# Performance work log

Measured on AMD Instinct MI355X. Metric: run time of the kernel, lower is better.

## Reference

```python
import jax, jax.numpy as jnp
import numpy as np

LN_EPS = 1e-5


def layer_norm(x, g, b):
    m = jnp.mean(x, axis=-1, keepdims=True)
    v = jnp.mean(jnp.square(x - m), axis=-1, keepdims=True)
    return (x - m) * jax.lax.rsqrt(v + LN_EPS) * g + b


def sym_norm(A):
    # D^{-1/2} (A + I) D^{-1/2}
    N = A.shape[0]
    Ah = A + jnp.eye(N, dtype=A.dtype)
    d = jnp.sum(Ah, axis=-1)
    dinv = jax.lax.rsqrt(jnp.maximum(d, 1e-12))
    return Ah * dinv[:, None] * dinv[None, :]


def gru_layer(xs, Wih, Whh, bih, bhh):
    # xs: (BN, T, Din) -> ys: (BN, T, H). PyTorch GRU cell math.
    BN, T, _ = xs.shape
    H = Whh.shape[1]
    x_proj = xs @ Wih.T + bih  # (BN, T, 3H), precompute input projections

    def step(h, xp):
        hp = h @ Whh.T + bhh
        xr, xz, xn = jnp.split(xp, 3, axis=-1)
        hr, hz, hn = jnp.split(hp, 3, axis=-1)
        r = jax.nn.sigmoid(xr + hr)
        z = jax.nn.sigmoid(xz + hz)
        n = jnp.tanh(xn + r * hn)
        h_new = (1.0 - z) * n + z * h
        return h_new, h_new

    h0 = jnp.zeros((BN, H), xs.dtype)
    _, ys = jax.lax.scan(step, h0, jnp.swapaxes(x_proj, 0, 1))
    return jnp.swapaxes(ys, 0, 1)


def amscf_forward(x, A, FSP, DSP,
                  E1, E2, fus_W, fus_b, fus_v, beta1, beta2,
                  gcn_W1, gcn_b1, ln1_g, ln1_b, gcn_W2, gcn_b2, ln2_g, ln2_b,
                  gru_Wih0, gru_Whh0, gru_bih0, gru_bhh0,
                  gru_Wih1, gru_Whh1, gru_bih1, gru_bhh1,
                  att_w, fc1_W, fc1_b, fc2_W, fc2_b):
    B, T, N, _ = x.shape
    Hor = fc2_W.shape[0]

    # ImprovedAdjacency: blend A with adaptive node-embedding adjacency
    Aadp = jax.nn.softmax(jax.nn.relu(E1 @ E2.T), axis=-1)
    IA = 0.5 * A + 0.5 * Aadp

    # fuse_with_A with learned gates
    w1 = jax.nn.sigmoid(beta1)
    w2 = jax.nn.sigmoid(beta2)
    C1 = w1 * A + (1.0 - w1) * FSP
    C2 = w2 * A + (1.0 - w2) * DSP

    # TransposeAttentionFusion: graph-level attention over the 3 candidate graphs
    Gs = jnp.stack([IA, C1, C2], axis=0)  # (3, N, N)
    sc = jnp.mean(jnp.tanh(Gs @ fus_W.T + fus_b) @ fus_v, axis=-1)  # (3,)
    alpha = jax.nn.softmax(sc)
    MG = jnp.einsum('k,knm->nm', alpha, Gs)

    S_hat = sym_norm(MG)  # (N, N)

    # TwoLayerGCN over all (B, T) at once: act(LN(S X W1)) -> LN(S h W2)
    xf = x.reshape(B * T, N, 1)
    h = jnp.einsum('mn,bnc->bmc', S_hat, xf) @ gcn_W1 + gcn_b1
    h = jax.nn.relu(layer_norm(h, ln1_g, ln1_b))
    g = jnp.einsum('mn,bnc->bmc', S_hat, h) @ gcn_W2 + gcn_b2
    g = layer_norm(g, ln2_g, ln2_b)  # (B*T, N, C)

    C = g.shape[-1]
    # Faithful to original: raw view of (B, T, N, C) into (B*N, T, C)
    H_seq = g.reshape(B, T, N, C).reshape(B * N, T, C)

    out = gru_layer(H_seq, gru_Wih0, gru_Whh0, gru_bih0, gru_bhh0)
    out = gru_layer(out, gru_Wih1, gru_Whh1, gru_bih1, gru_bhh1)  # (BN, T, Hg)

    # SoftAttentionPooling over time
    score = out @ att_w  # (BN, T)
    att = jax.nn.softmax(score, axis=1)
    ctx = jnp.einsum('bt,bth->bh', att, out)

    hfc = jax.nn.gelu(ctx @ fc1_W.T + fc1_b)
    dlt = hfc @ fc2_W.T + fc2_b  # (BN, Hor); dropout is identity at eval
    return jnp.transpose(dlt.reshape(B, N, Hor), (0, 2, 1))  # (B, Hor, N)


def setup_inputs() -> dict:
    B, T, N, Hor = 32, 12, 1000, 12
    Cin, Ch, Cout, Hg, Da, De = 1, 96, 96, 192, 32, 10
    key = jax.random.key(0)
    ks = jax.random.split(key, 32)
    f32 = jnp.float32

    def nrm(k, shape, scale):
        return jax.random.normal(k, shape, dtype=f32) * scale

    inp = {
        'x': jax.random.normal(ks[0], (B, T, N, Cin), dtype=f32),
        'A': jax.random.uniform(ks[1], (N, N), dtype=f32),
        'FSP': jax.random.uniform(ks[2], (N, N), dtype=f32),
        'DSP': jax.random.uniform(ks[3], (N, N), dtype=f32),
        'E1': nrm(ks[4], (N, De), 0.1),
        'E2': nrm(ks[5], (N, De), 0.1),
        'fus_W': nrm(ks[6], (Da, N), 1.0 / np.sqrt(N)),
        'fus_b': jnp.zeros((Da,), f32),
        'fus_v': nrm(ks[7], (Da,), 1.0 / np.sqrt(Da)),
        'beta1': jnp.float32(0.5),
        'beta2': jnp.float32(0.5),
        'gcn_W1': nrm(ks[8], (Cin, Ch), 1.0 / np.sqrt(Cin)),
        'gcn_b1': jnp.zeros((Ch,), f32),
        'ln1_g': jnp.ones((Ch,), f32),
        'ln1_b': jnp.zeros((Ch,), f32),
        'gcn_W2': nrm(ks[9], (Ch, Cout), 1.0 / np.sqrt(Ch)),
        'gcn_b2': jnp.zeros((Cout,), f32),
        'ln2_g': jnp.ones((Cout,), f32),
        'ln2_b': jnp.zeros((Cout,), f32),
        'gru_Wih0': nrm(ks[10], (3 * Hg, Cout), 1.0 / np.sqrt(Hg)),
        'gru_Whh0': nrm(ks[11], (3 * Hg, Hg), 1.0 / np.sqrt(Hg)),
        'gru_bih0': jnp.zeros((3 * Hg,), f32),
        'gru_bhh0': jnp.zeros((3 * Hg,), f32),
        'gru_Wih1': nrm(ks[12], (3 * Hg, Hg), 1.0 / np.sqrt(Hg)),
        'gru_Whh1': nrm(ks[13], (3 * Hg, Hg), 1.0 / np.sqrt(Hg)),
        'gru_bih1': jnp.zeros((3 * Hg,), f32),
        'gru_bhh1': jnp.zeros((3 * Hg,), f32),
        'att_w': nrm(ks[14], (Hg,), 1.0 / np.sqrt(Hg)),
        'fc1_W': nrm(ks[15], (Hg, Hg), 1.0 / np.sqrt(Hg)),
        'fc1_b': jnp.zeros((Hg,), f32),
        'fc2_W': nrm(ks[16], (Hor, Hg), 1.0 / np.sqrt(Hg)),
        'fc2_b': jnp.zeros((Hor,), f32),
    }
    return inp


def reference(x, A, FSP, DSP, E1, E2, fus_W, fus_b, fus_v, beta1, beta2,
              gcn_W1, gcn_b1, ln1_g, ln1_b, gcn_W2, gcn_b2, ln2_g, ln2_b,
              gru_Wih0, gru_Whh0, gru_bih0, gru_bhh0,
              gru_Wih1, gru_Whh1, gru_bih1, gru_bhh1,
              att_w, fc1_W, fc1_b, fc2_W, fc2_b):
    return amscf_forward(x, A, FSP, DSP, E1, E2, fus_W, fus_b, fus_v, beta1, beta2,
                         gcn_W1, gcn_b1, ln1_g, ln1_b, gcn_W2, gcn_b2, ln2_g, ln2_b,
                         gru_Wih0, gru_Whh0, gru_bih0, gru_bhh0,
                         gru_Wih1, gru_Whh1, gru_bih1, gru_bhh1,
                         att_w, fc1_W, fc1_b, fc2_W, fc2_b)
```

## Files before the change

### kernel.cpp

```cpp
#include <hip/hip_runtime.h>

typedef unsigned short u16;
typedef unsigned int u32;
typedef __attribute__((ext_vector_type(8))) short short8;
typedef __attribute__((ext_vector_type(4))) float float4v;

#define DEV static __device__ __forceinline__

DEV float bf2f(u16 u) { u32 x = ((u32)u) << 16; float f; __builtin_memcpy(&f, &x, 4); return f; }
DEV u16 f2bf(float f) {
  u32 u; __builtin_memcpy(&u, &f, 4);
  u = (u + 0x7fffu + ((u >> 16) & 1u)) >> 16;
  return (u16)u;
}
DEV float sigm(float x) { return 1.f / (1.f + __expf(-x)); }

DEV void gl16(const u16* g, u16* l) {
  __builtin_amdgcn_global_load_lds(
      (const __attribute__((address_space(1))) void*)g,
      (__attribute__((address_space(3))) void*)l, 16, 0, 0);
}

template <int OMODE>
__launch_bounds__(256)
__global__ void gemm_nt(const u16* __restrict__ A, int lda,
                        const u16* __restrict__ B, int ldb,
                        void* __restrict__ Cp, int ldc,
                        int M, int N, int K,
                        const float* __restrict__ bias)
{
  constexpr int PK = 40;
  __shared__ u16 As[128 * PK];
  __shared__ u16 Bs[64 * PK];

  const int tid  = threadIdx.x;
  const int m0   = blockIdx.y * 128;
  const int n0   = blockIdx.x * 64;
  const int wid  = tid >> 6;
  const int lane = tid & 63;
  const int l15  = lane & 15;
  const int quad = lane >> 4;
  const int wm   = (wid >> 1) * 64;
  const int wn   = (wid & 1) * 32;

  float4v acc[4][2];
  const float4v fz = {0.f, 0.f, 0.f, 0.f};
#pragma unroll
  for (int i = 0; i < 4; i++)
#pragma unroll
    for (int j = 0; j < 2; j++) acc[i][j] = fz;

  const int arow = tid >> 2;
  const int akc  = tid & 3;

  const int kt_count = (K + 31) / 32;
  for (int kt = 0; kt < kt_count; ++kt) {
    const int k0 = kt * 32 + akc * 8;
    const bool kok = (k0 < K);
    uint4 av0 = make_uint4(0, 0, 0, 0), av1 = av0, bv = av0;
    int ra = m0 + arow;
    if (kok && ra < M)        av0 = *(const uint4*)(A + (size_t)ra * lda + k0);
    if (kok && ra + 64 < M)   av1 = *(const uint4*)(A + (size_t)(ra + 64) * lda + k0);
    int rb = n0 + arow;
    if (kok && rb < N)        bv  = *(const uint4*)(B + (size_t)rb * ldb + k0);

    __syncthreads();
    *(uint4*)&As[arow * PK + akc * 8]        = av0;
    *(uint4*)&As[(arow + 64) * PK + akc * 8] = av1;
    *(uint4*)&Bs[arow * PK + akc * 8]        = bv;
    __syncthreads();

    short8 af[4], bfr[2];
#pragma unroll
    for (int i = 0; i < 4; i++)
      af[i] = *(const short8*)&As[(wm + i * 16 + l15) * PK + quad * 8];
#pragma unroll
    for (int j = 0; j < 2; j++)
      bfr[j] = *(const short8*)&Bs[(wn + j * 16 + l15) * PK + quad * 8];
#pragma unroll
    for (int i = 0; i < 4; i++)
#pragma unroll
      for (int j = 0; j < 2; j++)
        acc[i][j] = __builtin_amdgcn_mfma_f32_16x16x32_bf16(af[i], bfr[j], acc[i][j], 0, 0, 0);
  }

#pragma unroll
  for (int i = 0; i < 4; i++)
#pragma unroll
    for (int j = 0; j < 2; j++)
#pragma unroll
      for (int e = 0; e < 4; e++) {
        int r = m0 + wm + i * 16 + quad * 4 + e;
        int c = n0 + wn + j * 16 + l15;
        if (r < M && c < N) {
          float v = acc[i][j][e];
          if (OMODE == 0) ((float*)Cp)[(size_t)r * ldc + c] = v;
          else {
            float a = v + bias[c];
            float t = tanhf(0.7978845608028654f * (a + 0.044715f * a * a * a));
            ((float*)Cp)[(size_t)r * ldc + c] = 0.5f * a * (1.f + t);
          }
        }
      }
}

__launch_bounds__(256)
__global__ void k_bigemm(const u16* __restrict__ A,
                         const u16* __restrict__ B,
                         u16* __restrict__ Gg)
{
  __shared__ u16 As[128 * 32];
  __shared__ u16 Bs[128 * 32];
  const int tid  = threadIdx.x;
  const int bid  = blockIdx.x;
  const int xcd  = bid & 7;
  const int jj   = bid >> 3;
  const int m0   = (jj & 7) * 128;
  const int n0   = (xcd + 8 * (jj >> 3)) * 128;

  const int wid  = tid >> 6;
  const int lane = tid & 63;
  const int l15  = lane & 15;
  const int quad = lane >> 4;
  const int wm   = (wid >> 1) * 64;
  const int wn   = (wid & 1) * 64;

  const int srow = wid * 16 + (lane >> 2);
  const int skc  = (((lane & 3) ^ ((lane >> 2) & 3))) * 8;

  const u16* agp0 = A + (size_t)(m0 + srow) * 1024 + skc;
  const u16* agp1 = agp0 + (size_t)64 * 1024;
  const u16* bgp0 = B + (size_t)(n0 + srow) * 1024 + skc;
  const u16* bgp1 = bgp0 + (size_t)64 * 1024;
  u16* asl0 = &As[(wid * 16) * 32];
  u16* asl1 = &As[(64 + wid * 16) * 32];
  u16* bsl0 = &Bs[(wid * 16) * 32];
  u16* bsl1 = &Bs[(64 + wid * 16) * 32];

  float4v acc[4][4];
  const float4v fz = {0.f, 0.f, 0.f, 0.f};
#pragma unroll
  for (int i = 0; i < 4; i++)
#pragma unroll
    for (int j = 0; j < 4; j++) acc[i][j] = fz;

  const int swa = (quad ^ (l15 & 3)) * 8;

  for (int kt = 0; kt < 32; ++kt) {
    const int ko = kt * 32;
    gl16(agp0 + ko, asl0);
    gl16(agp1 + ko, asl1);
    gl16(bgp0 + ko, bsl0);
    gl16(bgp1 + ko, bsl1);
    __syncthreads();
    short8 af[4], bf[4];
#pragma unroll
    for (int i = 0; i < 4; i++)
      af[i] = *(const short8*)&As[(wm + i * 16 + l15) * 32 + swa];
#pragma unroll
    for (int j = 0; j < 4; j++)
      bf[j] = *(const short8*)&Bs[(wn + j * 16 + l15) * 32 + swa];
#pragma unroll
    for (int i = 0; i < 4; i++)
#pragma unroll
      for (int j = 0; j < 4; j++)
        acc[i][j] = __builtin_amdgcn_mfma_f32_16x16x32_bf16(af[i], bf[j], acc[i][j], 0, 0, 0);
    __syncthreads();
  }

#pragma unroll
  for (int i = 0; i < 4; i++)
#pragma unroll
    for (int j = 0; j < 4; j++)
#pragma unroll
      for (int e = 0; e < 4; e++) {
        int r = m0 + wm + i * 16 + quad * 4 + e;
        if (r < 1000) {
          int c = n0 + wn + j * 16 + l15;
          int rs = c / 96, cc = c - rs * 96;
          Gg[(size_t)rs * 96000 + (size_t)r * 96 + cc] = f2bf(acc[i][j][e]);
        }
      }
}

template <int KX, bool POOL>
__launch_bounds__(256)
__global__ void k_gru(const u16* __restrict__ Xin, int ldx,
                      const u16* __restrict__ Win,
                      const u16* __restrict__ Hin,
                      const u16* __restrict__ Whh,
                      const float* __restrict__ bih, const float* __restrict__ bhh,
                      u16* __restrict__ Hout,
                      const float* __restrict__ att_w, float* __restrict__ score,
                      int t0)
{
  __shared__ u16 As[128 * 64];
  __shared__ u16 Bs[96 * 64];
  const int tid  = threadIdx.x;
  const int m0   = blockIdx.y * 128;
  const int c0   = blockIdx.x * 32;
  const int wid  = tid >> 6;
  const int lane = tid & 63;
  const int l15  = lane & 15;
  const int quad = lane >> 4;
  const int wm   = wid * 32;

  const int srow8 = lane >> 3;
  const int sw8   = ((lane & 7) ^ srow8) * 8;
  const int srow4 = lane >> 2;
  const int sw4   = (((lane & 3) ^ (srow4 & 3))) * 8;

  float4v aR[2][2], aZ[2][2], aXN[2][2], aHN[2][2];
  const float4v fz = {0.f, 0.f, 0.f, 0.f};
#pragma unroll
  for (int i = 0; i < 2; i++)
#pragma unroll
    for (int j = 0; j < 2; j++) { aR[i][j] = fz; aZ[i][j] = fz; aXN[i][j] = fz; aHN[i][j] = fz; }

  if (KX == 96) {
    const u16* ax0 = Xin + (size_t)(m0 + wid * 16 + srow4) * ldx + sw4;
    const u16* ax1 = Xin + (size_t)(m0 + 64 + wid * 16 + srow4) * ldx + sw4;
    const int b0 = wid * 16 + srow4;
    const u16* bx0 = Win + (size_t)((b0 >> 5) * 192 + c0 + (b0 & 31)) * 96 + sw4;
    const int b1 = 64 + wid * 16 + srow4;
    const u16* bx1 = Win + (size_t)(384 + c0 + (b1 & 31)) * 96 + sw4;
    u16* asl0 = &As[(wid * 16) * 32];
    u16* asl1 = &As[(64 + wid * 16) * 32];
    u16* bsl0 = &Bs[(wid * 16) * 32];
    u16* bsl1 = &Bs[(64 + wid * 16) * 32];
    const int swa = (quad ^ (l15 & 3)) * 8;
#pragma unroll
    for (int kt = 0; kt < 3; ++kt) {
      const int ko = kt * 32;
      gl16(ax0 + ko, asl0); gl16(ax1 + ko, asl1);
      gl16(bx0 + ko, bsl0);
      if (wid < 2) gl16(bx1 + ko, bsl1);
      __syncthreads();
      short8 af[2], bR[2], bZ[2], bN[2];
#pragma unroll
      for (int i = 0; i < 2; i++)
        af[i] = *(const short8*)&As[(wm + i * 16 + l15) * 32 + swa];
#pragma unroll
      for (int j = 0; j < 2; j++) {
        bR[j] = *(const short8*)&Bs[(j * 16 + l15) * 32 + swa];
        bZ[j] = *(const short8*)&Bs[(32 + j * 16 + l15) * 32 + swa];
        bN[j] = *(const short8*)&Bs[(64 + j * 16 + l15) * 32 + swa];
      }
#pragma unroll
      for (int i = 0; i < 2; i++)
#pragma unroll
        for (int j = 0; j < 2; j++) {
          aR[i][j]  = __builtin_amdgcn_mfma_f32_16x16x32_bf16(af[i], bR[j], aR[i][j], 0, 0, 0);
          aZ[i][j]  = __builtin_amdgcn_mfma_f32_16x16x32_bf16(af[i], bZ[j], aZ[i][j], 0, 0, 0);
          aXN[i][j] = __builtin_amdgcn_mfma_f32_16x16x32_bf16(af[i], bN[j], aXN[i][j], 0, 0, 0);
        }
      __syncthreads();
    }
  } else {
    const u16* abase = Xin + (size_t)(m0 + wid * 8 + srow8) * 192 + sw8;
    const u16* bbase = Win + (size_t)(c0 + wid * 8 + srow8) * 192 + sw8;
#pragma unroll
    for (int kt = 0; kt < 3; ++kt) {
      const int ko = kt * 64;
#pragma unroll
      for (int c = 0; c < 4; c++)
        gl16(abase + (size_t)c * 32 * 192 + ko, &As[(c * 32 + wid * 8) * 64]);
#pragma unroll
      for (int c = 0; c < 3; c++)
        gl16(bbase + (size_t)c * 192 * 192 + ko, &Bs[(c * 32 + wid * 8) * 64]);
      __syncthreads();
#pragma unroll
      for (int k32 = 0; k32 < 2; k32++) {
        const int swr = ((quad + 4 * k32) ^ (l15 & 7)) * 8;
        short8 af[2], bR[2], bZ[2], bN[2];
#pragma unroll
        for (int i = 0; i < 2; i++)
          af[i] = *(const short8*)&As[(wm + i * 16 + l15) * 64 + swr];
#pragma unroll
        for (int j = 0; j < 2; j++) {
          bR[j] = *(const short8*)&Bs[(j * 16 + l15) * 64 + swr];
          bZ[j] = *(const short8*)&Bs[(32 + j * 16 + l15) * 64 + swr];
          bN[j] = *(const short8*)&Bs[(64 + j * 16 + l15) * 64 + swr];
        }
#pragma unroll
        for (int i = 0; i < 2; i++)
#pragma unroll
          for (int j = 0; j < 2; j++) {
            aR[i][j]  = __builtin_amdgcn_mfma_f32_16x16x32_bf16(af[i], bR[j], aR[i][j], 0, 0, 0);
            aZ[i][j]  = __builtin_amdgcn_mfma_f32_16x16x32_bf16(af[i], bZ[j], aZ[i][j], 0, 0, 0);
            aXN[i][j] = __builtin_amdgcn_mfma_f32_16x16x32_bf16(af[i], bN[j], aXN[i][j], 0, 0, 0);
          }
      }
      __syncthreads();
    }
  }
  if (!t0) {
    const u16* abase = Hin + (size_t)(m0 + wid * 8 + srow8) * 192 + sw8;
    const u16* bbase = Whh + (size_t)(c0 + wid * 8 + srow8) * 192 + sw8;
#pragma unroll
    for (int kt = 0; kt < 3; ++kt) {
      const int ko = kt * 64;
#pragma unroll
      for (int c = 0; c < 4; c++)
        gl16(abase + (size_t)c * 32 * 192 + ko, &As[(c * 32 + wid * 8) * 64]);
#pragma unroll
      for (int c = 0; c < 3; c++)
        gl16(bbase + (size_t)c * 192 * 192 + ko, &Bs[(c * 32 + wid * 8) * 64]);
      __syncthreads();
#pragma unroll
      for (int k32 = 0; k32 < 2; k32++) {
        const int swr = ((quad + 4 * k32) ^ (l15 & 7)) * 8;
        short8 af[2], bR[2], bZ[2], bN[2];
#pragma unroll
        for (int i = 0; i < 2; i++)
          af[i] = *(const short8*)&As[(wm + i * 16 + l15) * 64 + swr];
#pragma unroll
        for (int j = 0; j < 2; j++) {
          bR[j] = *(const short8*)&Bs[(j * 16 + l15) * 64 + swr];
          bZ[j] = *(const short8*)&Bs[(32 + j * 16 + l15) * 64 + swr];
          bN[j] = *(const short8*)&Bs[(64 + j * 16 + l15) * 64 + swr];
        }
#pragma unroll
        for (int i = 0; i < 2; i++)
#pragma unroll
          for (int j = 0; j < 2; j++) {
            aR[i][j]  = __builtin_amdgcn_mfma_f32_16x16x32_bf16(af[i], bR[j], aR[i][j], 0, 0, 0);
            aZ[i][j]  = __builtin_amdgcn_mfma_f32_16x16x32_bf16(af[i], bZ[j], aZ[i][j], 0, 0, 0);
            aHN[i][j] = __builtin_amdgcn_mfma_f32_16x16x32_bf16(af[i], bN[j], aHN[i][j], 0, 0, 0);
          }
      }
      __syncthreads();
    }
  }

  float ps[2][4];
  if (POOL) {
#pragma unroll
    for (int i = 0; i < 2; i++)
#pragma unroll
      for (int e = 0; e < 4; e++) ps[i][e] = 0.f;
  }
#pragma unroll
  for (int j = 0; j < 2; ++j) {
    const int c = c0 + j * 16 + l15;
    const float brz = bih[c] + bhh[c];
    const float bzz = bih[192 + c] + bhh[192 + c];
    const float bxn = bih[384 + c];
    const float bhn = bhh[384 + c];
    const float aw  = POOL ? att_w[c] : 0.f;
#pragma unroll
    for (int i = 0; i < 2; ++i)
#pragma unroll
      for (int e = 0; e < 4; ++e) {
        const int row = m0 + wm + i * 16 + quad * 4 + e;
        float rg  = sigm(aR[i][j][e] + brz);
        float zg  = sigm(aZ[i][j][e] + bzz);
        float hnv = bhn + (t0 ? 0.f : aHN[i][j][e]);
        float ng  = tanhf(aXN[i][j][e] + bxn + rg * hnv);
        float hold = t0 ? 0.f : bf2f(Hin[(size_t)row * 192 + c]);
        float hnew = (1.f - zg) * ng + zg * hold;
        Hout[(size_t)row * 192 + c] = f2bf(hnew);
        if (POOL) ps[i][e] += hnew * aw;
      }
  }
  if (POOL) {
#pragma unroll
    for (int i = 0; i < 2; ++i)
#pragma unroll
      for (int e = 0; e < 4; ++e) {
        float v = ps[i][e];
        v += __shfl_xor(v, 1); v += __shfl_xor(v, 2);
        v += __shfl_xor(v, 4); v += __shfl_xor(v, 8);
        if (l15 == 0) atomicAdd(&score[m0 + wm + i * 16 + quad * 4 + e], v);
      }
  }
}

__launch_bounds__(256)
__global__ void k_pool(const u16* __restrict__ H, float* __restrict__ score,
                       float* __restrict__ Mbuf, float* __restrict__ Lbuf,
                       float* __restrict__ Nv, int t0)
{
  const int base = blockIdx.x * 1536;
  const int tid  = threadIdx.x;

  float prev[6], hnew[6], so[6], wn[6];
#pragma unroll
  for (int k = 0; k < 6; k++) {
    const int idx = base + tid + k * 256;
    const int q = idx / 192;
    const float s = score[q];
    hnew[k] = bf2f(H[idx]);
    if (t0) {
      so[k] = 0.f; wn[k] = 1.f; prev[k] = 0.f;
    } else {
      const float Mo = Mbuf[q];
      const float Mn = fmaxf(Mo, s);
      so[k] = __expf(Mo - Mn);
      wn[k] = __expf(s - Mn);
      prev[k] = Nv[idx];
    }
  }
  float Mw = 0.f, Lw = 0.f;
  int qw = -1;
  if (tid < 8) {
    qw = blockIdx.x * 8 + tid;
    const float s = score[qw];
    if (t0) { Mw = s; Lw = 1.f; }
    else {
      const float Mo = Mbuf[qw];
      const float Mn = fmaxf(Mo, s);
      Mw = Mn;
      Lw = Lbuf[qw] * __expf(Mo - Mn) + __expf(s - Mn);
    }
  }
  __syncthreads();
  if (tid < 8) { Mbuf[qw] = Mw; Lbuf[qw] = Lw; score[qw] = 0.f; }
#pragma unroll
  for (int k = 0; k < 6; k++) {
    const int idx = base + tid + k * 256;
    Nv[idx] = prev[k] * so[k] + wn[k] * hnew[k];
  }
}

__launch_bounds__(256)
__global__ void k_h2gemm(const float* __restrict__ yt, const float4* __restrict__ cwpk,
                         const u16* __restrict__ W2s, const float* __restrict__ consts,
                         u16* __restrict__ h2t)
{
  constexpr int PK = 40;
  __shared__ u16 As[128 * PK];
  __shared__ u16 Bs[96 * PK];
  __shared__ u16 Ts[96 * 136];

  const int tid  = threadIdx.x;
  const int m0   = blockIdx.x * 128;
  const int wid  = tid >> 6;
  const int lane = tid & 63;
  const int l15  = lane & 15;
  const int quad = lane >> 4;
  const int wm   = (wid >> 1) * 64;
  const int wn   = (wid & 1) * 48;

  const float P = consts[0], Q = consts[1], VW = consts[2], CWB = consts[3], VB = consts[4];

  const int arow = tid >> 2;
  const int akc  = tid & 3;

  float yv[2], mu[2], iv[2];
#pragma unroll
  for (int rr = 0; rr < 2; rr++) {
    int i = m0 + arow + rr * 64;
    int r = i / 1000, n = i - r * 1000;
    float y = yt[n * 384 + r];
    yv[rr] = y;
    mu[rr] = y * P + Q;
    iv[rr] = rsqrtf(y * y * VW + 2.f * y * CWB + VB + 1e-5f);
  }

  float4v acc[4][3];
  const float4v fz = {0.f, 0.f, 0.f, 0.f};
#pragma unroll
  for (int i = 0; i < 4; i++)
#pragma unroll
    for (int j = 0; j < 3; j++) acc[i][j] = fz;

  uint4 asave[2][3];
  const bool has2 = (arow < 32);

  for (int kt = 0; kt < 6; ++kt) {
    const int k0 = kt * 32 + akc * 8;
    uint4 av[2];
    if (kt < 3) {
#pragma unroll
      for (int rr = 0; rr < 2; rr++) {
        u16 hb[8];
#pragma unroll
        for (int e = 0; e < 8; e++) {
          float4 cw = cwpk[k0 + e];
          float t = yv[rr] * cw.x + cw.y - mu[rr];
          float h = fmaxf(t * iv[rr] * cw.z + cw.w, 0.f);
          hb[e] = f2bf(h);
        }
        __builtin_memcpy(&av[rr], hb, 16);
        asave[rr][kt] = av[rr];
      }
    } else {
      av[0] = asave[0][kt - 3];
      av[1] = asave[1][kt - 3];
    }
    uint4 bv0 = *(const uint4*)(W2s + (size_t)arow * 192 + k0);
    uint4 bv1 = make_uint4(0, 0, 0, 0);
    if (has2) bv1 = *(const uint4*)(W2s + (size_t)(arow + 64) * 192 + k0);

    __syncthreads();
    *(uint4*)&As[arow * PK + akc * 8]        = av[0];
    *(uint4*)&As[(arow + 64) * PK + akc * 8] = av[1];
    *(uint4*)&Bs[arow * PK + akc * 8]        = bv0;
    if (has2) *(uint4*)&Bs[(arow + 64) * PK + akc * 8] = bv1;
    __syncthreads();

    short8 af[4], bfr[3];
#pragma unroll
    for (int i = 0; i < 4; i++)
      af[i] = *(const short8*)&As[(wm + i * 16 + l15) * PK + quad * 8];
#pragma unroll
    for (int j = 0; j < 3; j++)
      bfr[j] = *(const short8*)&Bs[(wn + j * 16 + l15) * PK + quad * 8];
#pragma unroll
    for (int i = 0; i < 4; i++)
#pragma unroll
      for (int j = 0; j < 3; j++)
        acc[i][j] = __builtin_amdgcn_mfma_f32_16x16x32_bf16(af[i], bfr[j], acc[i][j], 0, 0, 0);
  }

#pragma unroll
  for (int i = 0; i < 4; i++)
#pragma unroll
    for (int j = 0; j < 3; j++)
#pragma unroll
      for (int e = 0; e < 4; e++) {
        int rowl = wm + i * 16 + quad * 4 + e;
        int c2   = wn + j * 16 + l15;
        Ts[c2 * 136 + rowl] = f2bf(acc[i][j][e]);
      }
  __syncthreads();
#pragma unroll
  for (int u = tid; u < 1536; u += 256) {
    int c2 = u >> 4, ch = u & 15;
    int iidx0 = m0 + ch * 8;
    int r = iidx0 / 1000, n0 = iidx0 - r * 1000;
    *(uint4*)(h2t + (size_t)(r * 96 + c2) * 1024 + n0) = *(const uint4*)&Ts[c2 * 136 + ch * 8];
  }
}

__launch_bounds__(256)
__global__ void k_prep(const float* x, const float* fus_W,
                       const float* Wih0, const float* Whh0,
                       const float* Wih1, const float* Whh1,
                       const float* gcn_W1, const float* gcn_b1,
                       const float* gcn_W2, const float* ln1g, const float* ln1b,
                       u16* xbf, u16* fusWbf, u16* Wih0b, u16* Whh0b, u16* Wih1b, u16* Whh1b,
                       u16* W2s, float4* cwpk, float* consts)
{
  long o = (long)blockIdx.x * 256 + threadIdx.x;
  if (o < 384000) xbf[o] = f2bf(x[o]);
  else if ((o -= 384000) < 32000) fusWbf[o] = f2bf(fus_W[o]);
  else if ((o -= 32000) < 55296)  Wih0b[o] = f2bf(Wih0[o]);
  else if ((o -= 55296) < 110592) Whh0b[o] = f2bf(Whh0[o]);
  else if ((o -= 110592) < 110592) Wih1b[o] = f2bf(Wih1[o]);
  else if ((o -= 110592) < 110592) Whh1b[o] = f2bf(Whh1[o]);
  else if ((o -= 110592) < 9216) {
    int c2 = (int)o / 96, c = (int)o - c2 * 96;
    float wv = gcn_W2[c * 96 + c2];
    u16 hi = f2bf(wv);
    u16 lo = f2bf(wv - bf2f(hi));
    W2s[c2 * 192 + c] = hi;
    W2s[c2 * 192 + 96 + c] = lo;
  }
  else if ((o -= 9216) < 96) {
    int c = (int)o;
    float4 cw;
    cw.x = gcn_W1[c]; cw.y = gcn_b1[c]; cw.z = ln1g[c]; cw.w = ln1b[c];
    cwpk[c] = cw;
  }
  if (blockIdx.x == 0 && threadIdx.x == 0) {
    float sw = 0, sb = 0, sww = 0, swb = 0, sbb = 0;
    for (int c = 0; c < 96; c++) {
      float wv = gcn_W1[c], b = gcn_b1[c];
      sw += wv; sb += b; sww += wv * wv; swb += wv * b; sbb += b * b;
    }
    float P = sw / 96.f, Q = sb / 96.f;
    consts[0] = P; consts[1] = Q;
    consts[2] = sww / 96.f - P * P;
    consts[3] = swb / 96.f - P * Q;
    consts[4] = sbb / 96.f - Q * Q;
  }
}

__launch_bounds__(256)
__global__ void k_zero(u16* __restrict__ h2t, float* __restrict__ score)
{
  int idx = blockIdx.x * 256 + threadIdx.x;
  if (idx < 110592) {
    int row = idx / 3, p = idx - row * 3;
    *(uint4*)(h2t + (size_t)row * 1024 + 1000 + p * 8) = make_uint4(0, 0, 0, 0);
  } else if ((idx -= 110592) < 32000) {
    score[idx] = 0.f;
  }
}

__launch_bounds__(256)
__global__ void k_w1split(const float* __restrict__ fc1W, u16* __restrict__ w1s)
{
  int idx = blockIdx.x * 256 + threadIdx.x;
  if (idx >= 192 * 192) return;
  int n = idx / 192, k = idx - n * 192;
  float w = fc1W[idx];
  u16 hi = f2bf(w);
  u16 lo = f2bf(w - bf2f(hi));
  w1s[(size_t)n * 576 + k]       = hi;
  w1s[(size_t)n * 576 + 192 + k] = lo;
  w1s[(size_t)n * 576 + 384 + k] = hi;
}

__launch_bounds__(256)
__global__ void k_adjrow(const float* __restrict__ A, const float* __restrict__ FSP,
                         const float* __restrict__ DSP, const float* __restrict__ E1,
                         const float* __restrict__ E2,
                         const float* beta1, const float* beta2,
                         u16* __restrict__ G, float* __restrict__ rowsums)
{
  __shared__ float z[1000];
  __shared__ float red[256];
  const int n = blockIdx.x, tid = threadIdx.x;

  float e1r[10];
#pragma unroll
  for (int d = 0; d < 10; d++) e1r[d] = E1[n * 10 + d];

  float lmax = -1e30f;
  for (int m = tid; m < 1000; m += 256) {
    float s = 0;
#pragma unroll
    for (int d = 0; d < 10; d++) s += e1r[d] * E2[m * 10 + d];
    s = fmaxf(s, 0.f);
    z[m] = s;
    lmax = fmaxf(lmax, s);
  }
  red[tid] = lmax; __syncthreads();
  for (int st = 128; st > 0; st >>= 1) { if (tid < st) red[tid] = fmaxf(red[tid], red[tid + st]); __syncthreads(); }
  const float mx = red[0]; __syncthreads();

  float lsum = 0;
  for (int m = tid; m < 1000; m += 256) { float e = __expf(z[m] - mx); z[m] = e; lsum += e; }
  red[tid] = lsum; __syncthreads();
  for (int st = 128; st > 0; st >>= 1) { if (tid < st) red[tid] += red[tid + st]; __syncthreads(); }
  const float inv = 1.f / red[0]; __syncthreads();

  const float w1 = sigm(beta1[0]);
  const float w2 = sigm(beta2[0]);
  float s0 = 0, s1 = 0, s2 = 0;
  for (int m = tid; m < 1000; m += 256) {
    float aadp = z[m] * inv;
    float a = A[n * 1000 + m], f = FSP[n * 1000 + m], dd = DSP[n * 1000 + m];
    float g0 = 0.5f * a + 0.5f * aadp;
    float g1 = w1 * a + (1.f - w1) * f;
    float g2 = w2 * a + (1.f - w2) * dd;
    G[0 * 1000000 + n * 1000 + m] = f2bf(g0);
    G[1 * 1000000 + n * 1000 + m] = f2bf(g1);
    G[2 * 1000000 + n * 1000 + m] = f2bf(g2);
    s0 += g0; s1 += g1; s2 += g2;
  }
  red[tid] = s0; __syncthreads();
  for (int st = 128; st > 0; st >>= 1) { if (tid < st) red[tid] += red[tid + st]; __syncthreads(); }
  if (tid == 0) rowsums[n] = red[0];
  __syncthreads();
  red[tid] = s1; __syncthreads();
  for (int st = 128; st > 0; st >>= 1) { if (tid < st) red[tid] += red[tid + st]; __syncthreads(); }
  if (tid == 0) rowsums[1000 + n] = red[0];
  __syncthreads();
  red[tid] = s2; __syncthreads();
  for (int st = 128; st > 0; st >>= 1) { if (tid < st) red[tid] += red[tid + st]; __syncthreads(); }
  if (tid == 0) rowsums[2000 + n] = red[0];
}

__launch_bounds__(256)
__global__ void k_sc(const float* __restrict__ P, const float* fus_b, const float* fus_v, float* sc)
{
  __shared__ float red[256];
  const int k = blockIdx.x, tid = threadIdx.x;
  float local = 0;
  for (int n = tid; n < 1000; n += 256) {
    const float* p = P + (size_t)(k * 1000 + n) * 32;
    float s = 0;
#pragma unroll
    for (int a = 0; a < 32; a++) s += tanhf(p[a] + fus_b[a]) * fus_v[a];
    local += s;
  }
  red[tid] = local; __syncthreads();
  for (int st = 128; st > 0; st >>= 1) { if (tid < st) red[tid] += red[tid + st]; __syncthreads(); }
  if (tid == 0) sc[k] = red[0] * (1.f / 1000.f);
}

__launch_bounds__(256)
__global__ void k_alpha(const float* sc, const float* rowsums, float* alpha_out, float* dinv)
{
  __shared__ float al[3];
  const int tid = threadIdx.x;
  if (tid == 0) {
    float m = fmaxf(sc[0], fmaxf(sc[1], sc[2]));
    float e0 = __expf(sc[0] - m), e1 = __expf(sc[1] - m), e2 = __expf(sc[2] - m);
    float inv = 1.f / (e0 + e1 + e2);
    al[0] = e0 * inv; al[1] = e1 * inv; al[2] = e2 * inv;
    alpha_out[0] = al[0]; alpha_out[1] = al[1]; alpha_out[2] = al[2];
  }
  __syncthreads();
  const float a0 = al[0], a1 = al[1], a2 = al[2];
  for (int n = tid; n < 1000; n += 256) {
    float d = a0 * rowsums[n] + a1 * rowsums[1000 + n] + a2 * rowsums[2000 + n] + 1.0f;
    dinv[n] = rsqrtf(fmaxf(d, 1e-12f));
  }
}

__launch_bounds__(256)
__global__ void k_shat(const u16* __restrict__ G, const float* alpha, const float* dinv,
                       u16* __restrict__ S)
{
  int idx = blockIdx.x * 256 + threadIdx.x;
  if (idx >= 1024000) return;
  int i = idx >> 10, j = idx & 1023;
  u16 val = 0;
  if (j < 1000) {
    const float a0 = alpha[0], a1 = alpha[1], a2 = alpha[2];
    int g = i * 1000 + j;
    float mg = a0 * bf2f(G[g]) + a1 * bf2f(G[1000000 + g]) + a2 * bf2f(G[2000000 + g]);
    if (i == j) mg += 1.0f;
    val = f2bf(mg * dinv[i] * dinv[j]);
  }
  S[(size_t)i * 1024 + j] = val;
}

__launch_bounds__(256)
__global__ void k_ln2g(u16* __restrict__ g, const float* __restrict__ b2,
                       const float* __restrict__ g2, const float* __restrict__ be2)
{
  const int i = blockIdx.x * 256 + threadIdx.x;
  if (i >= 384000) return;
  u16* row = g + (size_t)i * 96;

  uint4 raw[12];
#pragma unroll
  for (int t = 0; t < 12; t++) raw[t] = *(const uint4*)((const u16*)row + t * 8);

  float s = 0, ss = 0;
#pragma unroll
  for (int t = 0; t < 12; t++) {
    const u16* ch = (const u16*)&raw[t];
#pragma unroll
    for (int e = 0; e < 8; e++) {
      float v = bf2f(ch[e]) + b2[t * 8 + e];
      s += v; ss += v * v;
    }
  }
  const float mean = s * (1.f / 96.f);
  const float var  = ss * (1.f / 96.f) - mean * mean;
  const float isd  = rsqrtf(var + 1e-5f);

#pragma unroll
  for (int t = 0; t < 12; t++) {
    const u16* ch = (const u16*)&raw[t];
#pragma unroll
    for (int p = 0; p < 2; p++) {
      int c0 = t * 8 + p * 4;
      u32 w0 = f2bf((bf2f(ch[p * 4 + 0]) + b2[c0 + 0] - mean) * isd * g2[c0 + 0] + be2[c0 + 0]);
      u32 w1 = f2bf((bf2f(ch[p * 4 + 1]) + b2[c0 + 1] - mean) * isd * g2[c0 + 1] + be2[c0 + 1]);
      u32 w2 = f2bf((bf2f(ch[p * 4 + 2]) + b2[c0 + 2] - mean) * isd * g2[c0 + 2] + be2[c0 + 2]);
      u32 w3 = f2bf((bf2f(ch[p * 4 + 3]) + b2[c0 + 3] - mean) * isd * g2[c0 + 3] + be2[c0 + 3]);
      ((u32*)row)[t * 4 + p * 2 + 0] = (w0 | (w1 << 16));
      ((u32*)row)[t * 4 + p * 2 + 1] = (w2 | (w3 << 16));
    }
  }
}

__launch_bounds__(256)
__global__ void k_ctxsplit(const float* __restrict__ Nv, const float* __restrict__ Lbuf,
                           u16* __restrict__ ctxs)
{
  const int i = blockIdx.x * 256 + threadIdx.x;
  if (i >= 32000 * 192) return;
  const int q = i / 192, c = i - q * 192;
  float v = Nv[i] / Lbuf[q];
  u16 hi = f2bf(v);
  u16 lo = f2bf(v - bf2f(hi));
  u16* row = ctxs + (size_t)q * 576;
  row[c] = hi; row[192 + c] = hi; row[384 + c] = lo;
}

__launch_bounds__(192)
__global__ void k_fc2(const float* __restrict__ hfc, const float* __restrict__ fc2W,
                      const float* __restrict__ fc2b, float* __restrict__ out)
{
  __shared__ float w2S[12][193];
  __shared__ float hS[16][193];
  const int tid = threadIdx.x;
  const int q0 = blockIdx.x * 16;
  for (int idx = tid; idx < 12 * 192; idx += 192) {
    int o = idx / 192, k = idx - o * 192;
    w2S[o][k] = fc2W[idx];
  }
  for (int idx = tid; idx < 16 * 192; idx += 192) {
    int qq = idx / 192, k = idx - qq * 192;
    hS[qq][k] = hfc[(size_t)(q0 + qq) * 192 + k];
  }
  __syncthreads();
  const int qq = tid / 12, o = tid - qq * 12;
  float acc = fc2b[o];
#pragma unroll 8
  for (int k = 0; k < 192; k++) acc += hS[qq][k] * w2S[o][k];
  const int q = q0 + qq;
  const int b = q / 1000, node = q - b * 1000;
  out[(size_t)b * 12000 + o * 1000 + node] = acc;
}

extern "C" void kernel_launch(void* const* d_in, const int* in_sizes, int n_in,
                              void* d_out, int out_size, void* d_ws, size_t ws_size,
                              hipStream_t stream)
{
  const float* x     = (const float*)d_in[0];
  const float* A     = (const float*)d_in[1];
  const float* FSP   = (const float*)d_in[2];
  const float* DSP   = (const float*)d_in[3];
  const float* E1    = (const float*)d_in[4];
  const float* E2    = (const float*)d_in[5];
  const float* fus_W = (const float*)d_in[6];
  const float* fus_b = (const float*)d_in[7];
  const float* fus_v = (const float*)d_in[8];
  const float* beta1 = (const float*)d_in[9];
  const float* beta2 = (const float*)d_in[10];
  const float* gcn_W1= (const float*)d_in[11];
  const float* gcn_b1= (const float*)d_in[12];
  const float* ln1g  = (const float*)d_in[13];
  const float* ln1b  = (const float*)d_in[14];
  const float* gcn_W2= (const float*)d_in[15];
  const float* gcn_b2= (const float*)d_in[16];
  const float* ln2g  = (const float*)d_in[17];
  const float* ln2b  = (const float*)d_in[18];
  const float* Wih0  = (const float*)d_in[19];
  const float* Whh0  = (const float*)d_in[20];
  const float* bih0  = (const float*)d_in[21];
  const float* bhh0  = (const float*)d_in[22];
  const float* Wih1  = (const float*)d_in[23];
  const float* Whh1  = (const float*)d_in[24];
  const float* bih1  = (const float*)d_in[25];
  const float* bhh1  = (const float*)d_in[26];
  const float* att_w = (const float*)d_in[27];
  const float* fc1W  = (const float*)d_in[28];
  const float* fc1b  = (const float*)d_in[29];
  const float* fc2W  = (const float*)d_in[30];
  const float* fc2b  = (const float*)d_in[31];
  float* out = (float*)d_out;

  char* w = (char*)d_ws;
  auto alloc = [&](size_t bytes) -> char* {
    char* p = w;
    w += (bytes + 255) & ~(size_t)255;
    return p;
  };

  float* consts  = (float*)alloc(8 * 4);
  float* scp     = (float*)alloc(3 * 4);
  float* alphap  = (float*)alloc(3 * 4);
  float* rowsums = (float*)alloc(3000 * 4);
  float* dinvp   = (float*)alloc(1000 * 4);
  u16*   Gbuf    = (u16*)alloc((size_t)3000000 * 2);
  u16*   Sbf     = (u16*)alloc((size_t)1024 * 1024 * 2);
  u16*   xbf     = (u16*)alloc((size_t)384000 * 2);
  u16*   fusWbf  = (u16*)alloc((size_t)32000 * 2);
  u16*   Wih0b   = (u16*)alloc((size_t)55296 * 2);
  u16*   Whh0b   = (u16*)alloc((size_t)110592 * 2);
  u16*   Wih1b   = (u16*)alloc((size_t)110592 * 2);
  u16*   Whh1b   = (u16*)alloc((size_t)110592 * 2);
  u16*   w1s     = (u16*)alloc((size_t)192 * 576 * 2);
  u16*   W2s     = (u16*)alloc((size_t)96 * 192 * 2);
  float4* cwpk   = (float4*)alloc((size_t)96 * 16);
  float* Pbuf    = (float*)alloc((size_t)96000 * 4);
  float* yt      = (float*)alloc((size_t)384000 * 4);
  u16*   h2t     = (u16*)alloc((size_t)36864 * 1024 * 2);
  u16*   Gg      = (u16*)alloc((size_t)36864000 * 2);
  float* Nv      = (float*)alloc((size_t)6144000 * 4);
  float* Mbuf    = (float*)alloc((size_t)32000 * 4);
  float* Lbuf    = (float*)alloc((size_t)32000 * 4);
  float* score   = (float*)alloc((size_t)32000 * 4);

  u16* h0buf[2] = { h2t,                    h2t + (size_t)6144000 };
  u16* h1buf[2] = { h2t + (size_t)12288000, h2t + (size_t)18432000 };
  u16*   ctxs = h2t;
  float* hfc  = (float*)(h2t + (size_t)18432000);

  k_prep<<<3174, 256, 0, stream>>>(x, fus_W, Wih0, Whh0, Wih1, Whh1, gcn_W1, gcn_b1,
                                   gcn_W2, ln1g, ln1b,
                                   xbf, fusWbf, Wih0b, Whh0b, Wih1b, Whh1b, W2s, cwpk, consts);
  k_w1split<<<144, 256, 0, stream>>>(fc1W, w1s);
  k_zero<<<557, 256, 0, stream>>>(h2t, score);
  k_adjrow<<<1000, 256, 0, stream>>>(A, FSP, DSP, E1, E2, beta1, beta2, Gbuf, rowsums);
  gemm_nt<0><<<dim3(1, 24), 256, 0, stream>>>(Gbuf, 1000, fusWbf, 1000, Pbuf, 32, 3000, 32, 1000, nullptr);
  k_sc<<<3, 256, 0, stream>>>(Pbuf, fus_b, fus_v, scp);
  k_alpha<<<1, 256, 0, stream>>>(scp, rowsums, alphap, dinvp);
  k_shat<<<4000, 256, 0, stream>>>(Gbuf, alphap, dinvp, Sbf);
  gemm_nt<0><<<dim3(6, 8), 256, 0, stream>>>(Sbf, 1024, xbf, 1000, yt, 384, 1000, 384, 1000, nullptr);
  k_h2gemm<<<3000, 256, 0, stream>>>(yt, cwpk, W2s, consts, h2t);
  k_bigemm<<<2304, 256, 0, stream>>>(Sbf, h2t, Gg);
  k_ln2g<<<1500, 256, 0, stream>>>(Gg, gcn_b2, ln2g, ln2b);

  for (int t = 0; t < 12; ++t) {
    u16* h0in  = h0buf[t & 1];
    u16* h0out = h0buf[(t & 1) ^ 1];
    u16* h1in  = h1buf[t & 1];
    u16* h1out = h1buf[(t & 1) ^ 1];
    k_gru<96, false><<<dim3(6, 250), 256, 0, stream>>>(
        Gg + t * 96, 1152, Wih0b, h0in, Whh0b, bih0, bhh0, h0out, nullptr, nullptr, t == 0);
    k_gru<192, true><<<dim3(6, 250), 256, 0, stream>>>(
        h0out, 192, Wih1b, h1in, Whh1b, bih1, bhh1, h1out, att_w, score, t == 0);
    k_pool<<<4000, 256, 0, stream>>>(h1out, score, Mbuf, Lbuf, Nv, t == 0);
  }

  k_ctxsplit<<<24000, 256, 0, stream>>>(Nv, Lbuf, ctxs);
  gemm_nt<3><<<dim3(3, 250), 256, 0, stream>>>(ctxs, 576, w1s, 576, hfc, 192, 32000, 192, 576, fc1b);
  k_fc2<<<2000, 192, 0, stream>>>(hfc, fc2W, fc2b, out);
}
```

Baseline: 1.512 ms.

## Fuse LN2 into big GEMM epilogue and fold attention pooling into next GRU step

The big S·H GEMM now uses 96-wide column tiles matching one timestep so it can compute the LayerNorm (bias, mean, variance, affine) in its epilogue, removing the separate k_ln2g pass over Gg. The per-step k_pool launch is removed: the online-softmax pooling of the previous step's layer-1 output is done at the start of the next layer-0 GRU kernel, with score/M/L buffers double-buffered, and a single trailing pool pass remains for the final step. LDS swizzles were also adjusted. This cuts launches and a full read/write of Gg, at the cost of extra epilogue work, more grid blocks and trickier buffer-parity bookkeeping.

```diff
diff --git a/kernel.cpp b/kernel.cpp
--- a/kernel.cpp
+++ b/kernel.cpp
@@ -107,80 +107,120 @@
 __launch_bounds__(256)
 __global__ void k_bigemm(const u16* __restrict__ A,
                          const u16* __restrict__ B,
+                         const float* __restrict__ b2, const float* __restrict__ g2,
+                         const float* __restrict__ be2,
                          u16* __restrict__ Gg)
 {
   __shared__ u16 As[128 * 32];
-  __shared__ u16 Bs[128 * 32];
+  __shared__ u16 Bs[96 * 32];
+  __shared__ float stats[2][2][128];
+
   const int tid  = threadIdx.x;
   const int bid  = blockIdx.x;
   const int xcd  = bid & 7;
   const int jj   = bid >> 3;
   const int m0   = (jj & 7) * 128;
-  const int n0   = (xcd + 8 * (jj >> 3)) * 128;
+  const int rt   = xcd + 8 * (jj >> 3);
 
   const int wid  = tid >> 6;
   const int lane = tid & 63;
   const int l15  = lane & 15;
   const int quad = lane >> 4;
   const int wm   = (wid >> 1) * 64;
-  const int wn   = (wid & 1) * 64;
-
-  const int srow = wid * 16 + (lane >> 2);
-  const int skc  = (((lane & 3) ^ ((lane >> 2) & 3))) * 8;
-
-  const u16* agp0 = A + (size_t)(m0 + srow) * 1024 + skc;
+  const int wn   = (wid & 1) * 48;
+  const int wni  = wid & 1;
+
+  const int srow = lane >> 2;
+  const int skc  = ((lane & 3) ^ ((lane >> 3) & 3)) * 8;
+
+  const u16* agp0 = A + (size_t)(m0 + wid * 16 + srow) * 1024 + skc;
   const u16* agp1 = agp0 + (size_t)64 * 1024;
-  const u16* bgp0 = B + (size_t)(n0 + srow) * 1024 + skc;
+  const u16* bgp0 = B + (size_t)(rt * 96 + wid * 16 + srow) * 1024 + skc;
   const u16* bgp1 = bgp0 + (size_t)64 * 1024;
   u16* asl0 = &As[(wid * 16) * 32];
   u16* asl1 = &As[(64 + wid * 16) * 32];
   u16* bsl0 = &Bs[(wid * 16) * 32];
   u16* bsl1 = &Bs[(64 + wid * 16) * 32];
 
-  float4v acc[4][4];
+  float4v acc[4][3];
   const float4v fz = {0.f, 0.f, 0.f, 0.f};
 #pragma unroll
   for (int i = 0; i < 4; i++)
 #pragma unroll
-    for (int j = 0; j < 4; j++) acc[i][j] = fz;
-
-  const int swa = (quad ^ (l15 & 3)) * 8;
+    for (int j = 0; j < 3; j++) acc[i][j] = fz;
+
+  const int swa = (quad ^ ((l15 >> 1) & 3)) * 8;
 
   for (int kt = 0; kt < 32; ++kt) {
     const int ko = kt * 32;
     gl16(agp0 + ko, asl0);
     gl16(agp1 + ko, asl1);
     gl16(bgp0 + ko, bsl0);
-    gl16(bgp1 + ko, bsl1);
+    if (wid < 2) gl16(bgp1 + ko, bsl1);
     __syncthreads();
-    short8 af[4], bf[4];
+    short8 af[4], bf[3];
 #pragma unroll
     for (int i = 0; i < 4; i++)
       af[i] = *(const short8*)&As[(wm + i * 16 + l15) * 32 + swa];
 #pragma unroll
-    for (int j = 0; j < 4; j++)
+    for (int j = 0; j < 3; j++)
       bf[j] = *(const short8*)&Bs[(wn + j * 16 + l15) * 32 + swa];
 #pragma unroll
     for (int i = 0; i < 4; i++)
 #pragma unroll
-      for (int j = 0; j < 4; j++)
+      for (int j = 0; j < 3; j++)
         acc[i][j] = __builtin_amdgcn_mfma_f32_16x16x32_bf16(af[i], bf[j], acc[i][j], 0, 0, 0);
     __syncthreads();
   }
 
+  float b2v[3], g2v[3], bev[3];
+#pragma unroll
+  for (int j = 0; j < 3; j++) {
+    int c = wn + j * 16 + l15;
+    b2v[j] = b2[c]; g2v[j] = g2[c]; bev[j] = be2[c];
+  }
 #pragma unroll
   for (int i = 0; i < 4; i++)
 #pragma unroll
-    for (int j = 0; j < 4; j++)
-#pragma unroll
-      for (int e = 0; e < 4; e++) {
-        int r = m0 + wm + i * 16 + quad * 4 + e;
-        if (r < 1000) {
-          int c = n0 + wn + j * 16 + l15;
-          int rs = c / 96, cc = c - rs * 96;
-          Gg[(size_t)rs * 96000 + (size_t)r * 96 + cc] = f2bf(acc[i][j][e]);
+    for (int e = 0; e < 4; e++) {
+      float s = 0.f, ss = 0.f;
+#pragma unroll
+      for (int j = 0; j < 3; j++) {
+        float v = acc[i][j][e] + b2v[j];
+        acc[i][j][e] = v;
+        s += v; ss += v * v;
+      }
+      s += __shfl_xor(s, 1); ss += __shfl_xor(ss, 1);
+      s += __shfl_xor(s, 2); ss += __shfl_xor(ss, 2);
+      s += __shfl_xor(s, 4); ss += __shfl_xor(ss, 4);
+      s += __shfl_xor(s, 8); ss += __shfl_xor(ss, 8);
+      if (l15 == 0) {
+        int rl = wm + i * 16 + quad * 4 + e;
+        stats[wni][0][rl] = s;
+        stats[wni][1][rl] = ss;
+      }
+    }
+  __syncthreads();
+#pragma unroll
+  for (int i = 0; i < 4; i++)
+#pragma unroll
+    for (int e = 0; e < 4; e++) {
+      int rl = wm + i * 16 + quad * 4 + e;
+      int m = m0 + rl;
+      if (m < 1000) {
+        float ts  = stats[0][0][rl] + stats[1][0][rl];
+        float tss = stats[0][1][rl] + stats[1][1][rl];
+        float mean = ts * (1.f / 96.f);
+        float var  = tss * (1.f / 96.f) - mean * mean;
+        float isd  = rsqrtf(var + 1e-5f);
+#pragma unroll
+        for (int j = 0; j < 3; j++) {
+          int c = wn + j * 16 + l15;
+          Gg[(size_t)rt * 96000 + (size_t)m * 96 + c] =
+              f2bf((acc[i][j][e] - mean) * isd * g2v[j] + bev[j]);
         }
       }
+    }
 }
 
 template <int KX, bool POOL>
@@ -191,8 +231,15 @@
                       const u16* __restrict__ Whh,
                       const float* __restrict__ bih, const float* __restrict__ bhh,
                       u16* __restrict__ Hout,
-                      const float* __restrict__ att_w, float* __restrict__ score,
-                      int t0)
+                      const float* __restrict__ att_w,
+                      float* __restrict__ score_acc,
+                      float* __restrict__ score_zero,
+                      const u16* __restrict__ Hpool,
+                      const float* __restrict__ score_rd,
+                      const float* __restrict__ Mrd, const float* __restrict__ Lrd,
+                      float* __restrict__ Mwr, float* __restrict__ Lwr,
+                      float* __restrict__ Nvp,
+                      int t0, int pm)
 {
   __shared__ u16 As[128 * 64];
   __shared__ u16 Bs[96 * 64];
@@ -205,10 +252,42 @@
   const int quad = lane >> 4;
   const int wm   = wid * 32;
 
+  if (!POOL && pm) {
+#pragma unroll
+    for (int k = 0; k < 16; k++) {
+      int idx = k * 256 + tid;
+      int ql = idx >> 5, cl = idx & 31;
+      int q = m0 + ql, c = c0 + cl;
+      size_t nidx = (size_t)q * 192 + c;
+      float s = score_rd[q];
+      float hnew = bf2f(Hpool[nidx]);
+      float so, wnf, prev;
+      if (pm == 1) { so = 0.f; wnf = 1.f; prev = 0.f; }
+      else {
+        float Mo = Mrd[q];
+        float Mn = fmaxf(Mo, s);
+        so = __expf(Mo - Mn); wnf = __expf(s - Mn);
+        prev = Nvp[nidx];
+      }
+      Nvp[nidx] = prev * so + wnf * hnew;
+    }
+    if (blockIdx.x == 0 && tid < 128) {
+      int q = m0 + tid;
+      float s = score_rd[q];
+      if (pm == 1) { Mwr[q] = s; Lwr[q] = 1.f; }
+      else {
+        float Mo = Mrd[q], Mn = fmaxf(Mo, s);
+        Mwr[q] = Mn;
+        Lwr[q] = Lrd[q] * __expf(Mo - Mn) + __expf(s - Mn);
+      }
+    }
+  }
+  if (POOL && blockIdx.x == 0 && tid < 128) score_zero[m0 + tid] = 0.f;
+
   const int srow8 = lane >> 3;
   const int sw8   = ((lane & 7) ^ srow8) * 8;
   const int srow4 = lane >> 2;
-  const int sw4   = (((lane & 3) ^ (srow4 & 3))) * 8;
+  const int sw4   = ((lane & 3) ^ ((lane >> 3) & 3)) * 8;
 
   float4v aR[2][2], aZ[2][2], aXN[2][2], aHN[2][2];
   const float4v fz = {0.f, 0.f, 0.f, 0.f};
@@ -228,7 +307,7 @@
     u16* asl1 = &As[(64 + wid * 16) * 32];
     u16* bsl0 = &Bs[(wid * 16) * 32];
     u16* bsl1 = &Bs[(64 + wid * 16) * 32];
-    const int swa = (quad ^ (l15 & 3)) * 8;
+    const int swa = (quad ^ ((l15 >> 1) & 3)) * 8;
 #pragma unroll
     for (int kt = 0; kt < 3; ++kt) {
       const int ko = kt * 32;
@@ -371,55 +450,35 @@
         float v = ps[i][e];
         v += __shfl_xor(v, 1); v += __shfl_xor(v, 2);
         v += __shfl_xor(v, 4); v += __shfl_xor(v, 8);
-        if (l15 == 0) atomicAdd(&score[m0 + wm + i * 16 + quad * 4 + e], v);
-      }
-  }
-}
-
-__launch_bounds__(256)
-__global__ void k_pool(const u16* __restrict__ H, float* __restrict__ score,
-                       float* __restrict__ Mbuf, float* __restrict__ Lbuf,
-                       float* __restrict__ Nv, int t0)
+        if (l15 == 0) atomicAdd(&score_acc[m0 + wm + i * 16 + quad * 4 + e], v);
+      }
+  }
+}
+
+__launch_bounds__(256)
+__global__ void k_pool(const u16* __restrict__ H, const float* __restrict__ score_rd,
+                       const float* __restrict__ Mrd, const float* __restrict__ Lrd,
+                       float* __restrict__ Lwr, float* __restrict__ Nv)
 {
   const int base = blockIdx.x * 1536;
   const int tid  = threadIdx.x;
-
-  float prev[6], hnew[6], so[6], wn[6];
 #pragma unroll
   for (int k = 0; k < 6; k++) {
     const int idx = base + tid + k * 256;
     const int q = idx / 192;
-    const float s = score[q];
-    hnew[k] = bf2f(H[idx]);
-    if (t0) {
-      so[k] = 0.f; wn[k] = 1.f; prev[k] = 0.f;
-    } else {
-      const float Mo = Mbuf[q];
-      const float Mn = fmaxf(Mo, s);
-      so[k] = __expf(Mo - Mn);
-      wn[k] = __expf(s - Mn);
-      prev[k] = Nv[idx];
-    }
-  }
-  float Mw = 0.f, Lw = 0.f;
-  int qw = -1;
+    const float s = score_rd[q];
+    const float Mo = Mrd[q];
+    const float Mn = fmaxf(Mo, s);
+    const float so = __expf(Mo - Mn);
+    const float wn = __expf(s - Mn);
+    Nv[idx] = Nv[idx] * so + wn * bf2f(H[idx]);
+  }
   if (tid < 8) {
-    qw = blockIdx.x * 8 + tid;
-    const float s = score[qw];
-    if (t0) { Mw = s; Lw = 1.f; }
-    else {
-      const float Mo = Mbuf[qw];
-      const float Mn = fmaxf(Mo, s);
-      Mw = Mn;
-      Lw = Lbuf[qw] * __expf(Mo - Mn) + __expf(s - Mn);
-    }
-  }
-  __syncthreads();
-  if (tid < 8) { Mbuf[qw] = Mw; Lbuf[qw] = Lw; score[qw] = 0.f; }
-#pragma unroll
-  for (int k = 0; k < 6; k++) {
-    const int idx = base + tid + k * 256;
-    Nv[idx] = prev[k] * so[k] + wn[k] * hnew[k];
+    const int q = blockIdx.x * 8 + tid;
+    const float s = score_rd[q];
+    const float Mo = Mrd[q];
+    const float Mn = fmaxf(Mo, s);
+    Lwr[q] = Lrd[q] * __expf(Mo - Mn) + __expf(s - Mn);
   }
 }
 
@@ -579,14 +638,17 @@
 }
 
 __launch_bounds__(256)
-__global__ void k_zero(u16* __restrict__ h2t, float* __restrict__ score)
+__global__ void k_zero(u16* __restrict__ h2t, float* __restrict__ score0,
+                       float* __restrict__ score1)
 {
   int idx = blockIdx.x * 256 + threadIdx.x;
   if (idx < 110592) {
     int row = idx / 3, p = idx - row * 3;
     *(uint4*)(h2t + (size_t)row * 1024 + 1000 + p * 8) = make_uint4(0, 0, 0, 0);
   } else if ((idx -= 110592) < 32000) {
-    score[idx] = 0.f;
+    score0[idx] = 0.f;
+  } else if ((idx -= 32000) < 32000) {
+    score1[idx] = 0.f;
   }
 }
 
@@ -719,48 +781,6 @@
     val = f2bf(mg * dinv[i] * dinv[j]);
   }
   S[(size_t)i * 1024 + j] = val;
-}
-
-__launch_bounds__(256)
-__global__ void k_ln2g(u16* __restrict__ g, const float* __restrict__ b2,
-                       const float* __restrict__ g2, const float* __restrict__ be2)
-{
-  const int i = blockIdx.x * 256 + threadIdx.x;
-  if (i >= 384000) return;
-  u16* row = g + (size_t)i * 96;
-
-  uint4 raw[12];
-#pragma unroll
-  for (int t = 0; t < 12; t++) raw[t] = *(const uint4*)((const u16*)row + t * 8);
-
-  float s = 0, ss = 0;
-#pragma unroll
-  for (int t = 0; t < 12; t++) {
-    const u16* ch = (const u16*)&raw[t];
-#pragma unroll
-    for (int e = 0; e < 8; e++) {
-      float v = bf2f(ch[e]) + b2[t * 8 + e];
-      s += v; ss += v * v;
-    }
-  }
-  const float mean = s * (1.f / 96.f);
-  const float var  = ss * (1.f / 96.f) - mean * mean;
-  const float isd  = rsqrtf(var + 1e-5f);
-
-#pragma unroll
-  for (int t = 0; t < 12; t++) {
-    const u16* ch = (const u16*)&raw[t];
-#pragma unroll
-    for (int p = 0; p < 2; p++) {
-      int c0 = t * 8 + p * 4;
-      u32 w0 = f2bf((bf2f(ch[p * 4 + 0]) + b2[c0 + 0] - mean) * isd * g2[c0 + 0] + be2[c0 + 0]);
-      u32 w1 = f2bf((bf2f(ch[p * 4 + 1]) + b2[c0 + 1] - mean) * isd * g2[c0 + 1] + be2[c0 + 1]);
-      u32 w2 = f2bf((bf2f(ch[p * 4 + 2]) + b2[c0 + 2] - mean) * isd * g2[c0 + 2] + be2[c0 + 2]);
-      u32 w3 = f2bf((bf2f(ch[p * 4 + 3]) + b2[c0 + 3] - mean) * isd * g2[c0 + 3] + be2[c0 + 3]);
-      ((u32*)row)[t * 4 + p * 2 + 0] = (w0 | (w1 << 16));
-      ((u32*)row)[t * 4 + p * 2 + 1] = (w2 | (w3 << 16));
-    }
-  }
 }
 
 __launch_bounds__(256)
@@ -869,9 +889,15 @@
   u16*   h2t     = (u16*)alloc((size_t)36864 * 1024 * 2);
   u16*   Gg      = (u16*)alloc((size_t)36864000 * 2);
   float* Nv      = (float*)alloc((size_t)6144000 * 4);
-  float* Mbuf    = (float*)alloc((size_t)32000 * 4);
-  float* Lbuf    = (float*)alloc((size_t)32000 * 4);
-  float* score   = (float*)alloc((size_t)32000 * 4);
+  float* Mb0     = (float*)alloc((size_t)32000 * 4);
+  float* Mb1     = (float*)alloc((size_t)32000 * 4);
+  float* Lb0     = (float*)alloc((size_t)32000 * 4);
+  float* Lb1     = (float*)alloc((size_t)32000 * 4);
+  float* sc0     = (float*)alloc((size_t)32000 * 4);
+  float* sc1     = (float*)alloc((size_t)32000 * 4);
+  float* Mbuf[2] = { Mb0, Mb1 };
+  float* Lbuf[2] = { Lb0, Lb1 };
+  float* score[2]= { sc0, sc1 };
 
   u16* h0buf[2] = { h2t,                    h2t + (size_t)6144000 };
   u16* h1buf[2] = { h2t + (size_t)12288000, h2t + (size_t)18432000 };
@@ -882,7 +908,7 @@
                                    gcn_W2, ln1g, ln1b,
                                    xbf, fusWbf, Wih0b, Whh0b, Wih1b, Whh1b, W2s, cwpk, consts);
   k_w1split<<<144, 256, 0, stream>>>(fc1W, w1s);
-  k_zero<<<557, 256, 0, stream>>>(h2t, score);
+  k_zero<<<682, 256, 0, stream>>>(h2t, sc0, sc1);
   k_adjrow<<<1000, 256, 0, stream>>>(A, FSP, DSP, E1, E2, beta1, beta2, Gbuf, rowsums);
   gemm_nt<0><<<dim3(1, 24), 256, 0, stream>>>(Gbuf, 1000, fusWbf, 1000, Pbuf, 32, 3000, 32, 1000, nullptr);
   k_sc<<<3, 256, 0, stream>>>(Pbuf, fus_b, fus_v, scp);
@@ -890,22 +916,29 @@
   k_shat<<<4000, 256, 0, stream>>>(Gbuf, alphap, dinvp, Sbf);
   gemm_nt<0><<<dim3(6, 8), 256, 0, stream>>>(Sbf, 1024, xbf, 1000, yt, 384, 1000, 384, 1000, nullptr);
   k_h2gemm<<<3000, 256, 0, stream>>>(yt, cwpk, W2s, consts, h2t);
-  k_bigemm<<<2304, 256, 0, stream>>>(Sbf, h2t, Gg);
-  k_ln2g<<<1500, 256, 0, stream>>>(Gg, gcn_b2, ln2g, ln2b);
+  k_bigemm<<<3072, 256, 0, stream>>>(Sbf, h2t, gcn_b2, ln2g, ln2b, Gg);
 
   for (int t = 0; t < 12; ++t) {
     u16* h0in  = h0buf[t & 1];
     u16* h0out = h0buf[(t & 1) ^ 1];
     u16* h1in  = h1buf[t & 1];
     u16* h1out = h1buf[(t & 1) ^ 1];
+    const int pm = (t == 0) ? 0 : (t == 1 ? 1 : 2);
     k_gru<96, false><<<dim3(6, 250), 256, 0, stream>>>(
-        Gg + t * 96, 1152, Wih0b, h0in, Whh0b, bih0, bhh0, h0out, nullptr, nullptr, t == 0);
+        Gg + t * 96, 1152, Wih0b, h0in, Whh0b, bih0, bhh0, h0out,
+        nullptr, nullptr, nullptr,
+        h1in, score[(t + 1) & 1],
+        Mbuf[(t + 1) & 1], Lbuf[(t + 1) & 1], Mbuf[t & 1], Lbuf[t & 1],
+        Nv, t == 0, pm);
     k_gru<192, true><<<dim3(6, 250), 256, 0, stream>>>(
-        h0out, 192, Wih1b, h1in, Whh1b, bih1, bhh1, h1out, att_w, score, t == 0);
-    k_pool<<<4000, 256, 0, stream>>>(h1out, score, Mbuf, Lbuf, Nv, t == 0);
-  }
-
-  k_ctxsplit<<<24000, 256, 0, stream>>>(Nv, Lbuf, ctxs);
+        h0out, 192, Wih1b, h1in, Whh1b, bih1, bhh1, h1out,
+        att_w, score[t & 1], score[(t + 1) & 1],
+        nullptr, nullptr, nullptr, nullptr, nullptr, nullptr, nullptr,
+        t == 0, 0);
+  }
+  k_pool<<<4000, 256, 0, stream>>>(h1buf[0], score[1], Mbuf[1], Lbuf[1], Lbuf[0], Nv);
+
+  k_ctxsplit<<<24000, 256, 0, stream>>>(Nv, Lbuf[0], ctxs);
   gemm_nt<3><<<dim3(3, 250), 256, 0, stream>>>(ctxs, 576, w1s, 576, hfc, 192, 32000, 192, 576, fc1b);
   k_fc2<<<2000, 192, 0, stream>>>(hfc, fc2W, fc2b, out);
 }
```

Result: no change. 1.520 ms (+0.5%).
